# Optimization experiments

Measured on AMD Instinct MI355X. Metric: run time of the kernel, lower is better.

The kernel has to match this reference:

```python
import jax, jax.numpy as jnp
import numpy as np

B, T, IN, H, L = 16, 256, 256, 1024, 4

def setup_inputs() -> dict:
    key = jax.random.key(0)
    ks = jax.random.split(key, 5)
    return {
        "x": jax.random.normal(ks[0], (B, T, IN), jnp.float32),
        # gate axis order: 0=forget, 1=input-perc(sigmoid), 2=input-pot(tanh), 3=output
        "Wh": jax.random.normal(ks[1], (L, 4, H, H), jnp.float32) * 0.1,
        "Wx0": jax.random.normal(ks[2], (4, IN, H), jnp.float32) * 0.1,
        "Wx": jax.random.normal(ks[3], (L - 1, 4, H, H), jnp.float32) * 0.1,
        "b": jax.random.normal(ks[4], (L, 4, H), jnp.float32) * 0.1,
    }

def _run_layer(inp, wh, wx, bias):
    # inp: [B, T, D]; wh: [4, H, H]; wx: [4, D, H]; bias: [4, H]
    # Precompute all input projections for every timestep (time-major for scan).
    pre = jnp.einsum('btd,gdh->tbgh', inp, wx) + bias  # [T, B, 4, H]
    Bn = inp.shape[0]
    Hn = wh.shape[-1]

    def step(carry, px):
        h, c = carry  # short_term, long_term
        g = px + jnp.einsum('bh,gho->bgo', h, wh)  # [B, 4, H]
        f = jax.nn.sigmoid(g[:, 0])       # forget factor
        perc = jax.nn.sigmoid(g[:, 1])    # input gate (percent)
        pot = jnp.tanh(g[:, 2])           # input gate (potential)
        o = jax.nn.sigmoid(g[:, 3])       # output gate (uses OLD short_term)
        c_new = f * c + perc * pot
        h_new = jnp.tanh(c_new) * o
        return (h_new, c_new), h_new

    init = (jnp.zeros((Bn, Hn), inp.dtype), jnp.zeros((Bn, Hn), inp.dtype))
    (h, _), hs = jax.lax.scan(step, init, pre)
    return h, jnp.moveaxis(hs, 0, 1)  # final hidden [B,H], all hiddens [B,T,H]

def reference(x, Wh, Wx0, Wx, b):
    h, seq = _run_layer(x, Wh[0], Wx0, b[0])
    for i in range(1, Wh.shape[0]):
        h, seq = _run_layer(seq, Wh[i], Wx[i - 1], b[i])
    return h  # original returns (final_hidden, None); None dropped
```

## Files before the change

kernel.cpp:

```cpp
#include <hip/hip_runtime.h>


typedef float f32x4 __attribute__((ext_vector_type(4)));
typedef short bf16x8 __attribute__((ext_vector_type(8)));

__device__ __forceinline__ unsigned short f2bf_rn(float x) {
    unsigned int u = __float_as_uint(x);
    u += 0x7FFFu + ((u >> 16) & 1u);
    return (unsigned short)(u >> 16);
}
__device__ __forceinline__ float bf2f(unsigned short s) {
    return __uint_as_float(((unsigned int)s) << 16);
}
__device__ __forceinline__ float sigmoidf_(float x) { return 1.0f / (1.0f + __expf(-x)); }
__device__ __forceinline__ float tanhf_(float x) {
    float e = __expf(2.0f * x);
    return 1.0f - 2.0f / (e + 1.0f);
}

#define MFMA16(a, b, c) __builtin_amdgcn_mfma_f32_16x16x32_bf16((a), (b), (c), 0, 0, 0)

__global__ __launch_bounds__(256)
void pre_gemm(const float* __restrict__ A, const float* __restrict__ W,
              const float* __restrict__ bias, float* __restrict__ out, int K)
{
    __shared__ float As[16][132];
    __shared__ float Bs[16][132];

    const int tid = threadIdx.x;
    const int m0 = blockIdx.y << 7;
    const int n0 = blockIdx.x << 7;
    const int g  = n0 >> 10;
    const int jb = n0 & 1023;
    const float* Wg = W + (size_t)g * K * 1024 + jb;

    const int tx = tid & 15;
    const int ty = tid >> 4;
    const int alk = tid & 15;
    const int alm = tid >> 4;
    const int bln = tid & 127;
    const int blkk = tid >> 7;

    float acc[8][8];
#pragma unroll
    for (int i = 0; i < 8; ++i)
#pragma unroll
        for (int j = 0; j < 8; ++j) acc[i][j] = 0.f;

    for (int k0 = 0; k0 < K; k0 += 16) {
        __syncthreads();
#pragma unroll
        for (int r = 0; r < 8; ++r) {
            int m = alm + (r << 4);
            As[alk][m] = A[(size_t)(m0 + m) * K + (k0 + alk)];
        }
#pragma unroll
        for (int r = 0; r < 8; ++r) {
            int kk = blkk + (r << 1);
            Bs[kk][bln] = Wg[(size_t)(k0 + kk) * 1024 + bln];
        }
        __syncthreads();
#pragma unroll
        for (int k = 0; k < 16; ++k) {
            float a[8], bb[8];
            *(f32x4*)&a[0]  = *(const f32x4*)&As[k][ty << 2];
            *(f32x4*)&a[4]  = *(const f32x4*)&As[k][64 + (ty << 2)];
            *(f32x4*)&bb[0] = *(const f32x4*)&Bs[k][tx << 2];
            *(f32x4*)&bb[4] = *(const f32x4*)&Bs[k][64 + (tx << 2)];
#pragma unroll
            for (int i = 0; i < 8; ++i)
#pragma unroll
                for (int j = 0; j < 8; ++j)
                    acc[i][j] = fmaf(a[i], bb[j], acc[i][j]);
        }
    }

    float bj[8];
#pragma unroll
    for (int j = 0; j < 8; ++j) {
        int nloc = (j < 4) ? ((tx << 2) + j) : (64 + (tx << 2) + (j - 4));
        bj[j] = bias[n0 + nloc];
    }
#pragma unroll
    for (int i = 0; i < 8; ++i) {
        int mloc = (i < 4) ? ((ty << 2) + i) : (64 + (ty << 2) + (i - 4));
        int m = m0 + mloc;
        int bidx = m >> 8;
        int tt   = m & 255;
        float* orow = out + ((size_t)((tt << 4) + bidx) << 12) + n0;
#pragma unroll
        for (int j = 0; j < 8; ++j) {
            int nloc = (j < 4) ? ((tx << 2) + j) : (64 + (tx << 2) + (j - 4));
            orow[nloc] = acc[i][j] + bj[j];
        }
    }
}

__global__ __launch_bounds__(256)
void lstm_scan(const float* __restrict__ pre,
               const float* __restrict__ Wh,
               float* __restrict__ seq_out,
               unsigned short* __restrict__ hhi,
               unsigned short* __restrict__ hlo,
               int* __restrict__ ctr_l1,
               float* __restrict__ final_out,
               int is_last)
{
    const int wg   = blockIdx.x;
    const int tid  = threadIdx.x;
    const int wv   = tid >> 6;
    const int lane = tid & 63;
    const int bc   = lane & 15;
    const int quad = lane >> 4;

    __shared__ float red[4][64][4];
    __shared__ float gsh[16][17];

    const int g   = bc >> 2;
    const int col = (wg << 2) + (bc & 3);
    bf16x8 Whi[8], Wmi[8], Wlo[8];
#pragma unroll
    for (int ck = 0; ck < 8; ++ck) {
#pragma unroll
        for (int j = 0; j < 8; ++j) {
            int k = (wv << 8) + (ck << 5) + (quad << 3) + j;
            float w = Wh[((size_t)g << 20) + ((size_t)k << 10) + col];
            unsigned short hi = f2bf_rn(w);
            float r1 = w - bf2f(hi);
            unsigned short mi = f2bf_rn(r1);
            float r2 = r1 - bf2f(mi);
            unsigned short lo = f2bf_rn(r2);
            Whi[ck][j] = (short)hi;
            Wmi[ck][j] = (short)mi;
            Wlo[ck][j] = (short)lo;
        }
    }

    float creg = 0.f;
    int dead = 0;

    for (int t = 0; t < 256; ++t) {
        float pr[4];
        if (wv == 0) {
            const float* pp = pre + ((size_t)t << 16) + ((size_t)(bc >> 2) << 10)
                              + (wg << 2) + (bc & 3);
#pragma unroll
            for (int r = 0; r < 4; ++r)
                pr[r] = pp[(size_t)((quad << 2) + r) << 12];
        }

        if (t > 0 && wv == 0 && !dead) {
            const int* lb = ctr_l1 + (((t - 1) << 4) << 5);
            bool done = (lane >= 16);
            const int gi5 = (lane & 15) << 5;
            int guard = 0;
            for (;;) {
                if (!done)
                    done = __hip_atomic_load(lb + gi5, __ATOMIC_RELAXED,
                                             __HIP_MEMORY_SCOPE_AGENT) >= 16;
                if (__all(done)) break;
                __builtin_amdgcn_s_sleep(1);
                if (++guard > (1 << 15)) { dead = 1; break; }
            }
        }
        __syncthreads();
        asm volatile("" ::: "memory");

        f32x4 a00 = {0.f, 0.f, 0.f, 0.f};
        f32x4 a01 = a00, a10 = a00, a11 = a00;
        if (t > 0) {
            const size_t pb = ((size_t)(t - 1) << 14) + ((size_t)bc << 10) + (wv << 8);
            const unsigned short* ph = hhi + pb;
            const unsigned short* pl = hlo + pb;
            bf16x8 ahi[8], alo[8];
#pragma unroll
            for (int ck = 0; ck < 8; ++ck) {
                ahi[ck] = *(const bf16x8*)(ph + (ck << 5) + (quad << 3));
                alo[ck] = *(const bf16x8*)(pl + (ck << 5) + (quad << 3));
            }
#pragma unroll
            for (int ck = 0; ck < 8; ++ck) {
                if (ck & 1) {
                    a10 = MFMA16(ahi[ck], Whi[ck], a10);
                    a11 = MFMA16(ahi[ck], Wmi[ck], a11);
                    a10 = MFMA16(ahi[ck], Wlo[ck], a10);
                    a11 = MFMA16(alo[ck], Whi[ck], a11);
                    a10 = MFMA16(alo[ck], Wmi[ck], a10);
                } else {
                    a00 = MFMA16(ahi[ck], Whi[ck], a00);
                    a01 = MFMA16(ahi[ck], Wmi[ck], a01);
                    a00 = MFMA16(ahi[ck], Wlo[ck], a00);
                    a01 = MFMA16(alo[ck], Whi[ck], a01);
                    a00 = MFMA16(alo[ck], Wmi[ck], a00);
                }
            }
        }
        f32x4 acc = (a00 + a01) + (a10 + a11);
        *(f32x4*)&red[wv][lane][0] = acc;
        __syncthreads();

        if (wv == 0) {
            f32x4 s0 = *(const f32x4*)&red[0][lane][0];
            f32x4 s1 = *(const f32x4*)&red[1][lane][0];
            f32x4 s2 = *(const f32x4*)&red[2][lane][0];
            f32x4 s3 = *(const f32x4*)&red[3][lane][0];
            f32x4 s = (s0 + s1) + (s2 + s3);
#pragma unroll
            for (int r = 0; r < 4; ++r)
                gsh[(quad << 2) + r][bc] = s[r] + pr[r];

            const int b2 = lane >> 2, jl2 = lane & 3;
            float fg = sigmoidf_(gsh[b2][jl2]);
            float ig = sigmoidf_(gsh[b2][4 + jl2]);
            float pg = tanhf_(gsh[b2][8 + jl2]);
            float og = sigmoidf_(gsh[b2][12 + jl2]);
            creg = fg * creg + ig * pg;
            float h = tanhf_(creg) * og;

            const int j = (wg << 2) + jl2;
            unsigned short hh = f2bf_rn(h);
            unsigned short hl = f2bf_rn(h - bf2f(hh));
            size_t pidx = ((size_t)t << 14) + ((size_t)b2 << 10) + j;
            __hip_atomic_store(&hhi[pidx], hh, __ATOMIC_RELAXED, __HIP_MEMORY_SCOPE_AGENT);
            __hip_atomic_store(&hlo[pidx], hl, __ATOMIC_RELAXED, __HIP_MEMORY_SCOPE_AGENT);
            if (is_last && t == 255) final_out[((size_t)b2 << 10) + j] = h;

            __builtin_amdgcn_s_waitcnt(0);
            if (lane == 0)
                __hip_atomic_fetch_add(&ctr_l1[((t << 4) + (wg >> 4)) << 5], 1,
                                       __ATOMIC_RELAXED,
                                       __HIP_MEMORY_SCOPE_AGENT);

            if (!is_last)
                seq_out[((size_t)((b2 << 8) + t) << 10) + j] = h;
        }
    }
}

extern "C" void kernel_launch(void* const* d_in, const int* in_sizes, int n_in,
                              void* d_out, int out_size, void* d_ws, size_t ws_size,
                              hipStream_t stream)
{
    (void)in_sizes; (void)n_in; (void)out_size; (void)ws_size;

    const float* x    = (const float*)d_in[0];
    const float* Wh   = (const float*)d_in[1];
    const float* Wx0  = (const float*)d_in[2];
    const float* Wx   = (const float*)d_in[3];
    const float* bias = (const float*)d_in[4];

    float* pre  = (float*)d_ws;
    float* seqA = pre + 16777216;
    float* seqB = seqA + 4194304;
    unsigned short* hhi = (unsigned short*)(seqB + 4194304);
    unsigned short* hlo = hhi + 4194304;
    int* ctr = (int*)(hlo + 4194304);
    const size_t L1_PER_LAYER = 256 * 16 * 32;

    float* fout = (float*)d_out;

    hipMemsetAsync(ctr, 0, 4 * L1_PER_LAYER * sizeof(int), stream);

    const dim3 blk(256);
    const dim3 ggrid(32, 32);
    const size_t WLAYER = (size_t)4 * 1024 * 1024;

    for (int l = 0; l < 4; ++l) {
        const float* inp = (l == 0) ? x : ((l & 1) ? seqA : seqB);
        float* outp      = (l & 1) ? seqB : seqA;
        const float* wx  = (l == 0) ? Wx0 : (Wx + (size_t)(l - 1) * WLAYER);
        int K            = (l == 0) ? 256 : 1024;

        pre_gemm<<<ggrid, blk, 0, stream>>>(inp, wx, bias + (size_t)l * 4096, pre, K);

        const float* p = pre;
        const float* wh = Wh + (size_t)l * WLAYER;
        float* so = outp;
        unsigned short* phi = hhi;
        unsigned short* plo = hlo;
        int* pl1 = ctr + (size_t)l * L1_PER_LAYER;
        int last = (l == 3);
        void* args[] = { (void*)&p, (void*)&wh, (void*)&so, (void*)&phi,
                         (void*)&plo, (void*)&pl1, (void*)&fout, (void*)&last };
        hipLaunchCooperativeKernel((void*)lstm_scan, dim3(256), blk, args, 0, stream);
    }
}
```

Measured before the change: 6.853 ms.

## Fuse consecutive LSTM layer pairs into one wavefront-pipelined persistent kernel

Adds a persistent cooperative kernel that runs two stacked LSTM layers at once. Layer B lags layer A by two timesteps, and layer B's input projection is computed on the fly from layer A's hidden state. This halves the number of serial scan launches and removes two of the four pre_gemm passes. In exchange each thread holds three split-bf16 weight sets in registers, which adds a lot of register pressure and extra MFMA work per step. An occupancy check falls back to the old per-layer path if the kernel cannot be resident.

```diff
diff --git a/kernel.cpp b/kernel.cpp
--- a/kernel.cpp
+++ b/kernel.cpp
@@ -237,6 +237,247 @@
     }
 }
 
+__global__ __launch_bounds__(256)
+void lstm_pair(const float* __restrict__ preA,
+               const float* __restrict__ WhA,
+               const float* __restrict__ WhB,
+               const float* __restrict__ WxB,
+               const float* __restrict__ biasB,
+               float* __restrict__ seq_out,
+               unsigned short* __restrict__ hAhi, unsigned short* __restrict__ hAlo,
+               unsigned short* __restrict__ hBhi, unsigned short* __restrict__ hBlo,
+               int* __restrict__ ctrA,
+               int* __restrict__ ctrB,
+               float* __restrict__ final_out,
+               int is_last)
+{
+    const int wg   = blockIdx.x;
+    const int tid  = threadIdx.x;
+    const int wv   = tid >> 6;
+    const int lane = tid & 63;
+    const int bc   = lane & 15;
+    const int quad = lane >> 4;
+
+    __shared__ float red[3][4][64][4];
+    __shared__ float gsh[2][16][17];
+    __shared__ float ring[2][16][17];
+
+    const int g   = bc >> 2;
+    const int col = (wg << 2) + (bc & 3);
+
+    bf16x8 WAh[8], WAm[8], WAl[8];
+    bf16x8 WBh[8], WBm[8], WBl[8];
+    bf16x8 WXh[8], WXm[8], WXl[8];
+#pragma unroll
+    for (int ck = 0; ck < 8; ++ck) {
+#pragma unroll
+        for (int j = 0; j < 8; ++j) {
+            const int k = (wv << 8) + (ck << 5) + (quad << 3) + j;
+            const size_t widx = ((size_t)g << 20) + ((size_t)k << 10) + col;
+            {
+                float w = WhA[widx];
+                unsigned short hi = f2bf_rn(w); float r1 = w - bf2f(hi);
+                unsigned short mi = f2bf_rn(r1); float r2 = r1 - bf2f(mi);
+                WAh[ck][j] = (short)hi; WAm[ck][j] = (short)mi;
+                WAl[ck][j] = (short)f2bf_rn(r2);
+            }
+            {
+                float w = WhB[widx];
+                unsigned short hi = f2bf_rn(w); float r1 = w - bf2f(hi);
+                unsigned short mi = f2bf_rn(r1); float r2 = r1 - bf2f(mi);
+                WBh[ck][j] = (short)hi; WBm[ck][j] = (short)mi;
+                WBl[ck][j] = (short)f2bf_rn(r2);
+            }
+            {
+                float w = WxB[widx];
+                unsigned short hi = f2bf_rn(w); float r1 = w - bf2f(hi);
+                unsigned short mi = f2bf_rn(r1); float r2 = r1 - bf2f(mi);
+                WXh[ck][j] = (short)hi; WXm[ck][j] = (short)mi;
+                WXl[ck][j] = (short)f2bf_rn(r2);
+            }
+        }
+    }
+    const float biasv = biasB[((size_t)g << 10) + col];
+
+    float creg = 0.f;
+    int dead = 0;
+
+    for (int s = 0; s < 258; ++s) {
+        float pr[4];
+        if (wv == 0 && s < 256) {
+            const float* pp = preA + ((size_t)s << 16) + ((size_t)g << 10) + col;
+#pragma unroll
+            for (int r = 0; r < 4; ++r)
+                pr[r] = pp[(size_t)((quad << 2) + r) << 12];
+        }
+
+        if (s > 0 && wv == 0 && !dead) {
+            bool done;
+            const int gi = lane & 15;
+            const int* wp;
+            if (lane < 16)      { done = (s > 256); wp = ctrA + (((s - 1) << 4) + gi) * 32; }
+            else if (lane < 32) { done = (s < 3);   wp = ctrB + (((s - 1) << 4) + gi) * 32; }
+            else                { done = true;      wp = ctrA; }
+            int guard = 0;
+            for (;;) {
+                if (!done)
+                    done = __hip_atomic_load(wp, __ATOMIC_RELAXED,
+                                             __HIP_MEMORY_SCOPE_AGENT) >= 16;
+                if (__all(done)) break;
+                __builtin_amdgcn_s_sleep(1);
+                if (++guard > (1 << 14)) { dead = 1; break; }
+            }
+        }
+        __syncthreads();
+        asm volatile("" ::: "memory");
+
+        f32x4 aA0 = {0.f, 0.f, 0.f, 0.f}, aA1 = aA0;
+        f32x4 aP0 = aA0, aP1 = aA0;
+        f32x4 aB0 = aA0, aB1 = aA0;
+
+        if (s >= 1 && s <= 256) {
+            const size_t pb = ((size_t)(s - 1) << 14) + ((size_t)bc << 10) + (wv << 8);
+            const unsigned short* ph = hAhi + pb;
+            const unsigned short* pl = hAlo + pb;
+#pragma unroll
+            for (int ck = 0; ck < 8; ++ck) {
+                bf16x8 ah = *(const bf16x8*)(ph + (ck << 5) + (quad << 3));
+                bf16x8 al = *(const bf16x8*)(pl + (ck << 5) + (quad << 3));
+                if (ck & 1) {
+                    aA1 = MFMA16(ah, WAh[ck], aA1);
+                    aA1 = MFMA16(ah, WAm[ck], aA1);
+                    aA1 = MFMA16(ah, WAl[ck], aA1);
+                    aA1 = MFMA16(al, WAh[ck], aA1);
+                    aA1 = MFMA16(al, WAm[ck], aA1);
+                    aP1 = MFMA16(ah, WXh[ck], aP1);
+                    aP1 = MFMA16(ah, WXm[ck], aP1);
+                    aP1 = MFMA16(ah, WXl[ck], aP1);
+                    aP1 = MFMA16(al, WXh[ck], aP1);
+                    aP1 = MFMA16(al, WXm[ck], aP1);
+                } else {
+                    aA0 = MFMA16(ah, WAh[ck], aA0);
+                    aA0 = MFMA16(ah, WAm[ck], aA0);
+                    aA0 = MFMA16(ah, WAl[ck], aA0);
+                    aA0 = MFMA16(al, WAh[ck], aA0);
+                    aA0 = MFMA16(al, WAm[ck], aA0);
+                    aP0 = MFMA16(ah, WXh[ck], aP0);
+                    aP0 = MFMA16(ah, WXm[ck], aP0);
+                    aP0 = MFMA16(ah, WXl[ck], aP0);
+                    aP0 = MFMA16(al, WXh[ck], aP0);
+                    aP0 = MFMA16(al, WXm[ck], aP0);
+                }
+            }
+        }
+        if (s >= 3) {
+            const size_t pb = ((size_t)(s - 3) << 14) + ((size_t)bc << 10) + (wv << 8);
+            const unsigned short* ph = hBhi + pb;
+            const unsigned short* pl = hBlo + pb;
+#pragma unroll
+            for (int ck = 0; ck < 8; ++ck) {
+                bf16x8 bh = *(const bf16x8*)(ph + (ck << 5) + (quad << 3));
+                bf16x8 bl = *(const bf16x8*)(pl + (ck << 5) + (quad << 3));
+                if (ck & 1) {
+                    aB1 = MFMA16(bh, WBh[ck], aB1);
+                    aB1 = MFMA16(bh, WBm[ck], aB1);
+                    aB1 = MFMA16(bh, WBl[ck], aB1);
+                    aB1 = MFMA16(bl, WBh[ck], aB1);
+                    aB1 = MFMA16(bl, WBm[ck], aB1);
+                } else {
+                    aB0 = MFMA16(bh, WBh[ck], aB0);
+                    aB0 = MFMA16(bh, WBm[ck], aB0);
+                    aB0 = MFMA16(bh, WBl[ck], aB0);
+                    aB0 = MFMA16(bl, WBh[ck], aB0);
+                    aB0 = MFMA16(bl, WBm[ck], aB0);
+                }
+            }
+        }
+
+        *(f32x4*)&red[0][wv][lane][0] = aA0 + aA1;
+        *(f32x4*)&red[1][wv][lane][0] = aP0 + aP1;
+        *(f32x4*)&red[2][wv][lane][0] = aB0 + aB1;
+        __syncthreads();
+
+        if (wv == 0) {
+            if (s <= 255) {
+                f32x4 s0 = *(const f32x4*)&red[0][0][lane][0];
+                f32x4 s1 = *(const f32x4*)&red[0][1][lane][0];
+                f32x4 s2 = *(const f32x4*)&red[0][2][lane][0];
+                f32x4 s3 = *(const f32x4*)&red[0][3][lane][0];
+                f32x4 sm = (s0 + s1) + (s2 + s3);
+#pragma unroll
+                for (int r = 0; r < 4; ++r)
+                    gsh[0][(quad << 2) + r][bc] = sm[r] + pr[r];
+
+                const int b2 = lane >> 2, jl2 = lane & 3;
+                float fg = sigmoidf_(gsh[0][b2][jl2]);
+                float ig = sigmoidf_(gsh[0][b2][4 + jl2]);
+                float pg = tanhf_(gsh[0][b2][8 + jl2]);
+                float og = sigmoidf_(gsh[0][b2][12 + jl2]);
+                creg = fg * creg + ig * pg;
+                float h = tanhf_(creg) * og;
+                const int j = (wg << 2) + jl2;
+                unsigned short hh = f2bf_rn(h);
+                unsigned short hl = f2bf_rn(h - bf2f(hh));
+                size_t pidx = ((size_t)s << 14) + ((size_t)b2 << 10) + j;
+                __hip_atomic_store(&hAhi[pidx], hh, __ATOMIC_RELAXED, __HIP_MEMORY_SCOPE_AGENT);
+                __hip_atomic_store(&hAlo[pidx], hl, __ATOMIC_RELAXED, __HIP_MEMORY_SCOPE_AGENT);
+                __builtin_amdgcn_s_waitcnt(0);
+                if (lane == 0)
+                    __hip_atomic_fetch_add(&ctrA[((s << 4) + (wg >> 4)) << 5], 1,
+                                           __ATOMIC_RELAXED,
+                                           __HIP_MEMORY_SCOPE_AGENT);
+            }
+        } else if (wv == 1) {
+            if (s >= 2) {
+                const int t1 = s - 2;
+                f32x4 s0 = *(const f32x4*)&red[2][0][lane][0];
+                f32x4 s1 = *(const f32x4*)&red[2][1][lane][0];
+                f32x4 s2 = *(const f32x4*)&red[2][2][lane][0];
+                f32x4 s3 = *(const f32x4*)&red[2][3][lane][0];
+                f32x4 sm = (s0 + s1) + (s2 + s3);
+#pragma unroll
+                for (int r = 0; r < 4; ++r)
+                    gsh[1][(quad << 2) + r][bc] =
+                        sm[r] + ring[t1 & 1][(quad << 2) + r][bc];
+
+                const int b2 = lane >> 2, jl2 = lane & 3;
+                float fg = sigmoidf_(gsh[1][b2][jl2]);
+                float ig = sigmoidf_(gsh[1][b2][4 + jl2]);
+                float pg = tanhf_(gsh[1][b2][8 + jl2]);
+                float og = sigmoidf_(gsh[1][b2][12 + jl2]);
+                creg = fg * creg + ig * pg;
+                float h = tanhf_(creg) * og;
+                const int j = (wg << 2) + jl2;
+                unsigned short hh = f2bf_rn(h);
+                unsigned short hl = f2bf_rn(h - bf2f(hh));
+                size_t pidx = ((size_t)t1 << 14) + ((size_t)b2 << 10) + j;
+                __hip_atomic_store(&hBhi[pidx], hh, __ATOMIC_RELAXED, __HIP_MEMORY_SCOPE_AGENT);
+                __hip_atomic_store(&hBlo[pidx], hl, __ATOMIC_RELAXED, __HIP_MEMORY_SCOPE_AGENT);
+                __builtin_amdgcn_s_waitcnt(0);
+                if (lane == 0)
+                    __hip_atomic_fetch_add(&ctrB[((s << 4) + (wg >> 4)) << 5], 1,
+                                           __ATOMIC_RELAXED,
+                                           __HIP_MEMORY_SCOPE_AGENT);
+                if (!is_last)
+                    seq_out[((size_t)((b2 << 8) + t1) << 10) + j] = h;
+                if (is_last && t1 == 255)
+                    final_out[((size_t)b2 << 10) + j] = h;
+            }
+        } else if (wv == 2) {
+            if (s >= 1 && s <= 256) {
+                f32x4 q0 = *(const f32x4*)&red[1][0][lane][0];
+                f32x4 q1 = *(const f32x4*)&red[1][1][lane][0];
+                f32x4 q2 = *(const f32x4*)&red[1][2][lane][0];
+                f32x4 q3 = *(const f32x4*)&red[1][3][lane][0];
+                f32x4 qm = (q0 + q1) + (q2 + q3);
+#pragma unroll
+                for (int r = 0; r < 4; ++r)
+                    ring[(s - 1) & 1][(quad << 2) + r][bc] = qm[r] + biasv;
+            }
+        }
+    }
+}
+
 extern "C" void kernel_launch(void* const* d_in, const int* in_sizes, int n_in,
                               void* d_out, int out_size, void* d_ws, size_t ws_size,
                               hipStream_t stream)
@@ -251,37 +492,68 @@
 
     float* pre  = (float*)d_ws;
     float* seqA = pre + 16777216;
-    float* seqB = seqA + 4194304;
-    unsigned short* hhi = (unsigned short*)(seqB + 4194304);
-    unsigned short* hlo = hhi + 4194304;
-    int* ctr = (int*)(hlo + 4194304);
-    const size_t L1_PER_LAYER = 256 * 16 * 32;
+    float* reg2 = seqA + 4194304;
+    unsigned short* hAhi = (unsigned short*)(reg2 + 4194304);
+    unsigned short* hAlo = hAhi + 4194304;
+    int* ctr = (int*)(hAlo + 4194304);
+    const size_t PAIR_PL = 258 * 16 * 32;
+    const size_t FB_PL   = 256 * 16 * 32;
 
     float* fout = (float*)d_out;
-
-    hipMemsetAsync(ctr, 0, 4 * L1_PER_LAYER * sizeof(int), stream);
-
     const dim3 blk(256);
     const dim3 ggrid(32, 32);
     const size_t WLAYER = (size_t)4 * 1024 * 1024;
 
-    for (int l = 0; l < 4; ++l) {
-        const float* inp = (l == 0) ? x : ((l & 1) ? seqA : seqB);
-        float* outp      = (l & 1) ? seqB : seqA;
-        const float* wx  = (l == 0) ? Wx0 : (Wx + (size_t)(l - 1) * WLAYER);
-        int K            = (l == 0) ? 256 : 1024;
-
-        pre_gemm<<<ggrid, blk, 0, stream>>>(inp, wx, bias + (size_t)l * 4096, pre, K);
-
-        const float* p = pre;
-        const float* wh = Wh + (size_t)l * WLAYER;
-        float* so = outp;
-        unsigned short* phi = hhi;
-        unsigned short* plo = hlo;
-        int* pl1 = ctr + (size_t)l * L1_PER_LAYER;
-        int last = (l == 3);
-        void* args[] = { (void*)&p, (void*)&wh, (void*)&so, (void*)&phi,
-                         (void*)&plo, (void*)&pl1, (void*)&fout, (void*)&last };
-        hipLaunchCooperativeKernel((void*)lstm_scan, dim3(256), blk, args, 0, stream);
-    }
-}
+    int nb = 0;
+    if (hipOccupancyMaxActiveBlocksPerMultiprocessor(&nb, lstm_pair, 256, 0)
+        != hipSuccess) nb = 0;
+
+    hipMemsetAsync(ctr, 0, 4 * PAIR_PL * sizeof(int), stream);
+
+    if (nb >= 1) {
+        unsigned short* hBhi = (unsigned short*)reg2;
+        unsigned short* hBlo = hBhi + 4194304;
+
+        pre_gemm<<<ggrid, blk, 0, stream>>>(x, Wx0, bias, pre, 256);
+        for (int p01 = 0; p01 < 2; ++p01) {
+            const float* p   = pre;
+            const float* whA = Wh + (size_t)(2 * p01) * WLAYER;
+            const float* whB = Wh + (size_t)(2 * p01 + 1) * WLAYER;
+            const float* wxB = Wx + (size_t)(2 * p01) * WLAYER;
+            const float* bB  = bias + (size_t)(2 * p01 + 1) * 4096;
+            float* so = seqA;
+            int* cA = ctr + (size_t)(2 * p01) * PAIR_PL;
+            int* cB = cA + PAIR_PL;
+            int last = (p01 == 1);
+            void* args[] = { (void*)&p, (void*)&whA, (void*)&whB, (void*)&wxB,
+                             (void*)&bB, (void*)&so, (void*)&hAhi, (void*)&hAlo,
+                             (void*)&hBhi, (void*)&hBlo, (void*)&cA, (void*)&cB,
+                             (void*)&fout, (void*)&last };
+            hipLaunchCooperativeKernel((void*)lstm_pair, dim3(256), blk, args, 0, stream);
+            if (p01 == 0)
+                pre_gemm<<<ggrid, blk, 0, stream>>>(seqA, Wx + WLAYER,
+                                                    bias + 2 * 4096, pre, 1024);
+        }
+    } else {
+        float* seqB = reg2;
+        unsigned short* hhi = hAhi;
+        unsigned short* hlo = hAlo;
+        for (int l = 0; l < 4; ++l) {
+            const float* inp = (l == 0) ? x : ((l & 1) ? seqA : seqB);
+            float* outp      = (l & 1) ? seqB : seqA;
+            const float* wx  = (l == 0) ? Wx0 : (Wx + (size_t)(l - 1) * WLAYER);
+            int K            = (l == 0) ? 256 : 1024;
+
+            pre_gemm<<<ggrid, blk, 0, stream>>>(inp, wx, bias + (size_t)l * 4096, pre, K);
+
+            const float* p = pre;
+            const float* wh = Wh + (size_t)l * WLAYER;
+            float* so = outp;
+            int* pl1 = ctr + (size_t)l * FB_PL;
+            int last = (l == 3);
+            void* args[] = { (void*)&p, (void*)&wh, (void*)&so, (void*)&hhi,
+                             (void*)&hlo, (void*)&pl1, (void*)&fout, (void*)&last };
+            hipLaunchCooperativeKernel((void*)lstm_scan, dim3(256), blk, args, 0, stream);
+        }
+    }
+}
```

Result: no change. 6.887 ms (+0.5%).

## Fuse next layer's input projection into the recurrent scan kernel

Applied to the files above, without the earlier changes.

Adds a fused scan kernel that, after computing each timestep's hidden state, also runs the next layer's input projection on it with MFMA. The result is written into the pre buffer two steps behind, so the separate pre_gemm launches for layers 1-3 and the seqA/seqB round trips go away. The cost is that every workgroup keeps a second full set of three-way-split bf16 weights in registers, which can hurt occupancy or cause spills. It also does more work per step inside the latency-bound serial loop. The old path stays as a fallback when the occupancy query reports zero blocks.

```diff
diff --git a/kernel.cpp b/kernel.cpp
--- a/kernel.cpp
+++ b/kernel.cpp
@@ -237,6 +237,203 @@
     }
 }
 
+__global__ __launch_bounds__(256)
+void lstm_scan_fused(float* pre,
+               const float* __restrict__ Wh,
+               const float* __restrict__ WxN,
+               const float* __restrict__ biasN,
+               unsigned short* __restrict__ hhi,
+               unsigned short* __restrict__ hlo,
+               int* __restrict__ ctr_l1,
+               float* __restrict__ final_out,
+               int is_last, int has_next)
+{
+    const int wg   = blockIdx.x;
+    const int tid  = threadIdx.x;
+    const int wv   = tid >> 6;
+    const int lane = tid & 63;
+    const int bc   = lane & 15;
+    const int quad = lane >> 4;
+
+    __shared__ float red[4][64][4];
+    __shared__ float redP[2][4][64][4];
+    __shared__ float gsh[16][17];
+
+    const int g   = bc >> 2;
+    const int col = (wg << 2) + (bc & 3);
+    bf16x8 Whi[8], Wmi[8], Wlo[8];
+#pragma unroll
+    for (int ck = 0; ck < 8; ++ck) {
+#pragma unroll
+        for (int j = 0; j < 8; ++j) {
+            int k = (wv << 8) + (ck << 5) + (quad << 3) + j;
+            float w = Wh[((size_t)g << 20) + ((size_t)k << 10) + col];
+            unsigned short hi = f2bf_rn(w);
+            float r1 = w - bf2f(hi);
+            unsigned short mi = f2bf_rn(r1);
+            float r2 = r1 - bf2f(mi);
+            unsigned short lo = f2bf_rn(r2);
+            Whi[ck][j] = (short)hi;
+            Wmi[ck][j] = (short)mi;
+            Wlo[ck][j] = (short)lo;
+        }
+    }
+    bf16x8 WXh[8], WXm[8], WXl[8];
+    if (has_next) {
+#pragma unroll
+        for (int ck = 0; ck < 8; ++ck) {
+#pragma unroll
+            for (int j = 0; j < 8; ++j) {
+                int k = (wv << 8) + (ck << 5) + (quad << 3) + j;
+                float w = WxN[((size_t)g << 20) + ((size_t)k << 10) + col];
+                unsigned short hi = f2bf_rn(w);
+                float r1 = w - bf2f(hi);
+                unsigned short mi = f2bf_rn(r1);
+                float r2 = r1 - bf2f(mi);
+                unsigned short lo = f2bf_rn(r2);
+                WXh[ck][j] = (short)hi;
+                WXm[ck][j] = (short)mi;
+                WXl[ck][j] = (short)lo;
+            }
+        }
+    }
+    const float biasvN = biasN[((size_t)g << 10) + col];
+
+    float creg = 0.f;
+    int dead = 0;
+    const int smax = has_next ? 258 : 256;
+
+    for (int s = 0; s < smax; ++s) {
+        float pr[4];
+        if (wv == 0 && s < 256) {
+            const float* pp = pre + ((size_t)s << 16) + ((size_t)g << 10) + col;
+#pragma unroll
+            for (int r = 0; r < 4; ++r)
+                pr[r] = pp[(size_t)((quad << 2) + r) << 12];
+        }
+
+        if (s >= 1 && s <= 256 && wv == 0 && !dead) {
+            const int* lb = ctr_l1 + (((s - 1) << 4) << 5);
+            bool done = (lane >= 16);
+            const int gi5 = (lane & 15) << 5;
+            int guard = 0;
+            for (;;) {
+                if (!done)
+                    done = __hip_atomic_load(lb + gi5, __ATOMIC_RELAXED,
+                                             __HIP_MEMORY_SCOPE_AGENT) >= 16;
+                if (__all(done)) break;
+                __builtin_amdgcn_s_sleep(1);
+                if (++guard > (1 << 15)) { dead = 1; break; }
+            }
+        }
+        __syncthreads();
+        asm volatile("" ::: "memory");
+
+        f32x4 a00 = {0.f, 0.f, 0.f, 0.f};
+        f32x4 a01 = a00, a10 = a00, a11 = a00;
+        if (s >= 1 && s < 256) {
+            const size_t pb = ((size_t)(s - 1) << 14) + ((size_t)bc << 10) + (wv << 8);
+            const unsigned short* ph = hhi + pb;
+            const unsigned short* pl = hlo + pb;
+            bf16x8 ahi[8], alo[8];
+#pragma unroll
+            for (int ck = 0; ck < 8; ++ck) {
+                ahi[ck] = *(const bf16x8*)(ph + (ck << 5) + (quad << 3));
+                alo[ck] = *(const bf16x8*)(pl + (ck << 5) + (quad << 3));
+            }
+#pragma unroll
+            for (int ck = 0; ck < 8; ++ck) {
+                if (ck & 1) {
+                    a10 = MFMA16(ahi[ck], Whi[ck], a10);
+                    a11 = MFMA16(ahi[ck], Wmi[ck], a11);
+                    a10 = MFMA16(ahi[ck], Wlo[ck], a10);
+                    a11 = MFMA16(alo[ck], Whi[ck], a11);
+                    a10 = MFMA16(alo[ck], Wmi[ck], a10);
+                } else {
+                    a00 = MFMA16(ahi[ck], Whi[ck], a00);
+                    a01 = MFMA16(ahi[ck], Wmi[ck], a01);
+                    a00 = MFMA16(ahi[ck], Wlo[ck], a00);
+                    a01 = MFMA16(alo[ck], Whi[ck], a01);
+                    a00 = MFMA16(alo[ck], Wmi[ck], a00);
+                }
+            }
+        }
+        f32x4 acc = (a00 + a01) + (a10 + a11);
+        *(f32x4*)&red[wv][lane][0] = acc;
+        __syncthreads();
+
+        if (wv == 0 && s < 256) {
+            f32x4 s0 = *(const f32x4*)&red[0][lane][0];
+            f32x4 s1 = *(const f32x4*)&red[1][lane][0];
+            f32x4 s2 = *(const f32x4*)&red[2][lane][0];
+            f32x4 s3 = *(const f32x4*)&red[3][lane][0];
+            f32x4 sv = (s0 + s1) + (s2 + s3);
+#pragma unroll
+            for (int r = 0; r < 4; ++r)
+                gsh[(quad << 2) + r][bc] = sv[r] + pr[r];
+
+            const int b2 = lane >> 2, jl2 = lane & 3;
+            float fg = sigmoidf_(gsh[b2][jl2]);
+            float ig = sigmoidf_(gsh[b2][4 + jl2]);
+            float pg = tanhf_(gsh[b2][8 + jl2]);
+            float og = sigmoidf_(gsh[b2][12 + jl2]);
+            creg = fg * creg + ig * pg;
+            float h = tanhf_(creg) * og;
+
+            const int j = (wg << 2) + jl2;
+            unsigned short hh = f2bf_rn(h);
+            unsigned short hl = f2bf_rn(h - bf2f(hh));
+            size_t pidx = ((size_t)s << 14) + ((size_t)b2 << 10) + j;
+            __hip_atomic_store(&hhi[pidx], hh, __ATOMIC_RELAXED, __HIP_MEMORY_SCOPE_AGENT);
+            __hip_atomic_store(&hlo[pidx], hl, __ATOMIC_RELAXED, __HIP_MEMORY_SCOPE_AGENT);
+            if (is_last && s == 255) final_out[((size_t)b2 << 10) + j] = h;
+
+            __builtin_amdgcn_s_waitcnt(0);
+            if (lane == 0)
+                __hip_atomic_fetch_add(&ctr_l1[((s << 4) + (wg >> 4)) << 5], 1,
+                                       __ATOMIC_RELAXED,
+                                       __HIP_MEMORY_SCOPE_AGENT);
+        } else if (wv == 1 && has_next && s >= 2) {
+            f32x4 q0 = *(const f32x4*)&redP[(s - 1) & 1][0][lane][0];
+            f32x4 q1 = *(const f32x4*)&redP[(s - 1) & 1][1][lane][0];
+            f32x4 q2 = *(const f32x4*)&redP[(s - 1) & 1][2][lane][0];
+            f32x4 q3 = *(const f32x4*)&redP[(s - 1) & 1][3][lane][0];
+            f32x4 qm = (q0 + q1) + (q2 + q3);
+            float* pw = pre + ((size_t)(s - 2) << 16) + ((size_t)g << 10) + col;
+#pragma unroll
+            for (int r = 0; r < 4; ++r)
+                pw[(size_t)((quad << 2) + r) << 12] = qm[r] + biasvN;
+        }
+
+        if (has_next && s >= 1 && s <= 256) {
+            const size_t pb = ((size_t)(s - 1) << 14) + ((size_t)bc << 10) + (wv << 8);
+            const unsigned short* ph = hhi + pb;
+            const unsigned short* pl = hlo + pb;
+            f32x4 p00 = {0.f, 0.f, 0.f, 0.f};
+            f32x4 p01 = p00, p10 = p00, p11 = p00;
+#pragma unroll
+            for (int ck = 0; ck < 8; ++ck) {
+                bf16x8 ah = *(const bf16x8*)(ph + (ck << 5) + (quad << 3));
+                bf16x8 al = *(const bf16x8*)(pl + (ck << 5) + (quad << 3));
+                if (ck & 1) {
+                    p10 = MFMA16(ah, WXh[ck], p10);
+                    p11 = MFMA16(ah, WXm[ck], p11);
+                    p10 = MFMA16(ah, WXl[ck], p10);
+                    p11 = MFMA16(al, WXh[ck], p11);
+                    p10 = MFMA16(al, WXm[ck], p10);
+                } else {
+                    p00 = MFMA16(ah, WXh[ck], p00);
+                    p01 = MFMA16(ah, WXm[ck], p01);
+                    p00 = MFMA16(ah, WXl[ck], p00);
+                    p01 = MFMA16(al, WXh[ck], p01);
+                    p00 = MFMA16(al, WXm[ck], p00);
+                }
+            }
+            *(f32x4*)&redP[s & 1][wv][lane][0] = (p00 + p01) + (p10 + p11);
+        }
+    }
+}
+
 extern "C" void kernel_launch(void* const* d_in, const int* in_sizes, int n_in,
                               void* d_out, int out_size, void* d_ws, size_t ws_size,
                               hipStream_t stream)
@@ -255,33 +452,53 @@
     unsigned short* hhi = (unsigned short*)(seqB + 4194304);
     unsigned short* hlo = hhi + 4194304;
     int* ctr = (int*)(hlo + 4194304);
-    const size_t L1_PER_LAYER = 256 * 16 * 32;
+    const size_t FB_PL = 256 * 16 * 32;
 
     float* fout = (float*)d_out;
 
-    hipMemsetAsync(ctr, 0, 4 * L1_PER_LAYER * sizeof(int), stream);
+    hipMemsetAsync(ctr, 0, 4 * FB_PL * sizeof(int), stream);
 
     const dim3 blk(256);
     const dim3 ggrid(32, 32);
     const size_t WLAYER = (size_t)4 * 1024 * 1024;
 
-    for (int l = 0; l < 4; ++l) {
-        const float* inp = (l == 0) ? x : ((l & 1) ? seqA : seqB);
-        float* outp      = (l & 1) ? seqB : seqA;
-        const float* wx  = (l == 0) ? Wx0 : (Wx + (size_t)(l - 1) * WLAYER);
-        int K            = (l == 0) ? 256 : 1024;
-
-        pre_gemm<<<ggrid, blk, 0, stream>>>(inp, wx, bias + (size_t)l * 4096, pre, K);
-
-        const float* p = pre;
-        const float* wh = Wh + (size_t)l * WLAYER;
-        float* so = outp;
-        unsigned short* phi = hhi;
-        unsigned short* plo = hlo;
-        int* pl1 = ctr + (size_t)l * L1_PER_LAYER;
-        int last = (l == 3);
-        void* args[] = { (void*)&p, (void*)&wh, (void*)&so, (void*)&phi,
-                         (void*)&plo, (void*)&pl1, (void*)&fout, (void*)&last };
-        hipLaunchCooperativeKernel((void*)lstm_scan, dim3(256), blk, args, 0, stream);
-    }
-}
+    int nb = 0;
+    if (hipOccupancyMaxActiveBlocksPerMultiprocessor(&nb, lstm_scan_fused, 256, 0)
+        != hipSuccess) nb = 0;
+
+    if (nb >= 1) {
+        pre_gemm<<<ggrid, blk, 0, stream>>>(x, Wx0, bias, pre, 256);
+        for (int l = 0; l < 4; ++l) {
+            float* p        = pre;
+            const float* wh = Wh + (size_t)l * WLAYER;
+            const float* wxn = Wx + (size_t)((l < 3) ? l : 2) * WLAYER;
+            const float* bn  = bias + (size_t)((l < 3) ? (l + 1) : 3) * 4096;
+            int* pl1 = ctr + (size_t)l * FB_PL;
+            int last  = (l == 3);
+            int hnext = (l < 3);
+            void* args[] = { (void*)&p, (void*)&wh, (void*)&wxn, (void*)&bn,
+                             (void*)&hhi, (void*)&hlo, (void*)&pl1,
+                             (void*)&fout, (void*)&last, (void*)&hnext };
+            hipLaunchCooperativeKernel((void*)lstm_scan_fused, dim3(256), blk,
+                                       args, 0, stream);
+        }
+    } else {
+        for (int l = 0; l < 4; ++l) {
+            const float* inp = (l == 0) ? x : ((l & 1) ? seqA : seqB);
+            float* outp      = (l & 1) ? seqB : seqA;
+            const float* wx  = (l == 0) ? Wx0 : (Wx + (size_t)(l - 1) * WLAYER);
+            int K            = (l == 0) ? 256 : 1024;
+
+            pre_gemm<<<ggrid, blk, 0, stream>>>(inp, wx, bias + (size_t)l * 4096, pre, K);
+
+            const float* p = pre;
+            const float* wh = Wh + (size_t)l * WLAYER;
+            float* so = outp;
+            int* pl1 = ctr + (size_t)l * FB_PL;
+            int last = (l == 3);
+            void* args[] = { (void*)&p, (void*)&wh, (void*)&so, (void*)&hhi,
+                             (void*)&hlo, (void*)&pl1, (void*)&fout, (void*)&last };
+            hipLaunchCooperativeKernel((void*)lstm_scan, dim3(256), blk, args, 0, stream);
+        }
+    }
+}
```

New measurement: 6.828 ms. About the same (-0.4%).
